# Kernel tuning notes

Hardware: AMD Instinct MI355X
Metric: run time of the kernel (lower is better)

The kernel has to match this reference:

```python
import jax, jax.numpy as jnp
import numpy as np

TOPK = 9
NUM_CLASSES = 80
BG_INDEX = NUM_CLASSES
B, N_GT = 16, 32
N_LEVEL_BBOXES = (25600, 6400, 1600)  # strides 8/16/32 on a 1280x1280 image
M = sum(N_LEVEL_BBOXES)
EPS = 1e-9


def _make_boxes(key, lead_shape, img_size=1280.0):
    k1, k2 = jax.random.split(key)
    c = jax.random.uniform(k1, lead_shape + (2,), minval=32.0, maxval=img_size - 32.0)
    wh = jax.random.uniform(k2, lead_shape + (2,), minval=8.0, maxval=256.0)
    return jnp.concatenate([c - wh * 0.5, c + wh * 0.5], axis=-1)


def setup_inputs() -> dict:
    key = jax.random.key(0)
    ks = jax.random.split(key, 5)
    anchor_bboxes = _make_boxes(ks[0], (M,))
    gt_bboxes = _make_boxes(ks[1], (B, N_GT))
    gt_labels = jax.random.randint(ks[2], (B, N_GT, 1), 0, NUM_CLASSES)
    mask_gt = (jax.random.uniform(ks[3], (B, N_GT, 1)) < 0.8).astype(jnp.float32)
    pred_bboxes = _make_boxes(ks[4], (B, M))
    return {"anchor_bboxes": anchor_bboxes, "n_level_bboxes": N_LEVEL_BBOXES,
            "gt_bboxes": gt_bboxes, "gt_labels": gt_labels,
            "mask_gt": mask_gt, "pred_bboxes": pred_bboxes}


def pairwise_iou(box1, box2):
    # box1 [..., N, 4], box2 [..., M, 4] -> [..., N, M]
    b1 = box1[..., :, None, :]
    b2 = box2[..., None, :, :]
    lt = jnp.maximum(b1[..., :2], b2[..., :2])
    rb = jnp.minimum(b1[..., 2:], b2[..., 2:])
    inter = jnp.clip(rb - lt, 0.0).prod(-1)
    area1 = (b1[..., 2:] - b1[..., :2]).prod(-1)
    area2 = (b2[..., 2:] - b2[..., :2]).prod(-1)
    return inter / (area1 + area2 - inter + EPS)


def reference(anchor_bboxes, n_level_bboxes, gt_bboxes, gt_labels, mask_gt, pred_bboxes):
    bs, n_max = gt_bboxes.shape[0], gt_bboxes.shape[1]
    n_anchors = anchor_bboxes.shape[0]

    overlaps = pairwise_iou(gt_bboxes.reshape(-1, 4), anchor_bboxes).reshape(bs, n_max, n_anchors)
    gt_centers = (gt_bboxes[..., :2] + gt_bboxes[..., 2:]) * 0.5            # [B,N,2]
    anchor_points = (anchor_bboxes[:, :2] + anchor_bboxes[:, 2:]) * 0.5      # [M,2]
    distances = jnp.sqrt(((gt_centers[:, :, None, :] - anchor_points[None, None, :, :]) ** 2).sum(-1))
    distances = jax.lax.stop_gradient(distances)  # only feeds integer topk indices

    # ---- per-FPN-level topk candidate selection (dedup via scatter-count) ----
    mask_gt_b = mask_gt.astype(bool)                 # [B,N,1]
    b_ix = jnp.arange(bs)[:, None, None]
    n_ix = jnp.arange(n_max)[None, :, None]
    is_in_candidate_list, candidate_indices = [], []
    start = 0
    for L in n_level_bboxes:
        k = min(TOPK, L)
        d = jax.lax.dynamic_slice_in_dim(distances, start, L, axis=-1)
        _, idx = jax.lax.top_k(-d, k)                # [B,N,k] k smallest distances
        candidate_indices.append(idx + start)
        idx_m = jnp.where(mask_gt_b, idx, 0)
        cnt = jnp.zeros((bs, n_max, L), distances.dtype).at[b_ix, n_ix, idx_m].add(1.0)
        cnt = jnp.where(cnt > 1, 0.0, cnt)           # drop duplicated indices
        is_in_candidate_list.append(cnt)
        start += L
    is_in_candidate = jnp.concatenate(is_in_candidate_list, -1)   # [B,N,M]
    candidate_indices = jnp.concatenate(candidate_indices, -1)    # [B,N,k*l]

    # ---- dynamic IoU threshold = mean + std over candidate overlaps ----
    iou_candidates = jnp.where(is_in_candidate > 0, overlaps, 0.0)
    gathered = jnp.take_along_axis(iou_candidates, candidate_indices, axis=-1)
    thr = gathered.mean(-1, keepdims=True) + gathered.std(-1, keepdims=True, ddof=1)
    is_positive = jnp.where(iou_candidates > thr, is_in_candidate, 0.0)

    # ---- anchor centers strictly inside gt boxes ----
    deltas = jnp.concatenate([anchor_points[None, None] - gt_bboxes[:, :, None, :2],
                              gt_bboxes[:, :, None, 2:] - anchor_points[None, None]], -1)
    is_in_gts = (deltas.min(-1) > EPS).astype(overlaps.dtype)     # [B,N,M]

    mask_positive = is_positive * is_in_gts * mask_gt

    # ---- resolve anchors matched to multiple gts by highest overlap ----
    fg_mask = mask_positive.sum(-2)                               # [B,M]
    multi = fg_mask[:, None, :] > 1
    is_max = jax.nn.one_hot(overlaps.argmax(1), n_max, dtype=mask_positive.dtype).transpose(0, 2, 1)
    mask_positive = jnp.where(multi, is_max, mask_positive)
    fg_mask = mask_positive.sum(-2)
    target_gt_index = mask_positive.argmax(-2)                    # [B,M]

    # ---- gather targets ----
    target_labels = jnp.take_along_axis(gt_labels[..., 0], target_gt_index, axis=1)
    target_labels = jnp.where(fg_mask > 0, target_labels, BG_INDEX)
    target_bboxes = jnp.take_along_axis(gt_bboxes, target_gt_index[..., None], axis=1)  # [B,M,4]
    target_scores = jax.nn.one_hot(target_labels, NUM_CLASSES + 1, dtype=jnp.float32)[..., :NUM_CLASSES]

    # ---- soft-label scaling by predicted-box IoU ----
    ious = pairwise_iou(gt_bboxes, pred_bboxes) * mask_positive
    target_scores = target_scores * ious.max(-2)[..., None]
    return target_labels, target_bboxes, target_scores, fg_mask > 0
```

## Files before the change

kernel.cpp:

```cpp
#include <hip/hip_runtime.h>
#include <stdint.h>

#define NCLS 80
#define BGI 80
#define BB 16
#define NGT 32
#define MM 33600
#define EPSF 1e-9f
#define CAP 1024

__device__ __forceinline__ float iou_f(const float4 b1, const float4 b2) {
#pragma clang fp contract(off)
  float ltx = fmaxf(b1.x, b2.x);
  float lty = fmaxf(b1.y, b2.y);
  float rbx = fminf(b1.z, b2.z);
  float rby = fminf(b1.w, b2.w);
  float iw = fmaxf(rbx - ltx, 0.0f);
  float ih = fmaxf(rby - lty, 0.0f);
  float inter = iw * ih;
  float a1 = (b1.z - b1.x) * (b1.w - b1.y);
  float a2 = (b2.z - b2.x) * (b2.w - b2.y);
  return inter / (a1 + a2 - inter + EPSF);
}

__global__ __launch_bounds__(256) void k_prep(
    const float4* __restrict__ anchors, float2* __restrict__ centers,
    unsigned int* __restrict__ pk) {
#pragma clang fp contract(off)
  const int i = blockIdx.x * 256 + threadIdx.x;
  if (i < MM) {
    const float4 ab = anchors[i];
    centers[i] = make_float2((ab.x + ab.z) * 0.5f, (ab.y + ab.w) * 0.5f);
  }
  pk[i] = 0u;
}

__global__ __launch_bounds__(1024) void k_topk(
    const float4* __restrict__ anchors, const float2* __restrict__ centers,
    const float4* __restrict__ gtb, const float* __restrict__ maskgt,
    unsigned int* __restrict__ pk) {
#pragma clang fp contract(off)
  const int pair = blockIdx.x;
  if (maskgt[pair] == 0.0f) return;
  const int b = pair >> 5;
  const int g = pair & 31;
  const int tid = threadIdx.x;
  const int lane = tid & 63;
  const int wid = tid >> 6;
  const float4 gb = gtb[pair];
  const float gcx = (gb.x + gb.z) * 0.5f;
  const float gcy = (gb.y + gb.w) * 0.5f;

  __shared__ unsigned long long buf[CAP];
  __shared__ unsigned long long winners[27];
  __shared__ float s_wmin[16];
  __shared__ float s_T;
  __shared__ unsigned int s_cnt;

  const int LSTART[3] = {0, 25600, 32000};
  const int LLEN[3]   = {25600, 6400, 1600};

#pragma unroll
  for (int lev = 0; lev < 3; ++lev) {
    const int start = LSTART[lev];
    const int len = LLEN[lev];

    float mymin = 3.4e38f;
    for (int j = tid; j < len; j += 1024) {
      const float2 ac = centers[start + j];
      const float dx = gcx - ac.x;
      const float dy = gcy - ac.y;
      mymin = fminf(mymin, dx * dx + dy * dy);
    }
#pragma unroll
    for (int s = 32; s >= 1; s >>= 1)
      mymin = fminf(mymin, __shfl_xor(mymin, s, 64));
    if (lane == 0) s_wmin[wid] = mymin;
    if (tid == 0) s_cnt = 0u;
    __syncthreads();

    if (wid == 0 && lane < 16) {
      const float v = s_wmin[lane];
      int r = 0;
#pragma unroll
      for (int q = 0; q < 16; ++q) {
        const float o = s_wmin[q];
        r += (o < v) || (o == v && q < lane);
      }
      if (r == 8) s_T = sqrtf(v);
    }
    __syncthreads();
    const float T = s_T;

    for (int j = tid; j < len; j += 1024) {
      const float2 ac = centers[start + j];
      const float dx = gcx - ac.x;
      const float dy = gcy - ac.y;
      const float dist = sqrtf(dx * dx + dy * dy);
      if (dist <= T) {
        const unsigned int p = atomicAdd(&s_cnt, 1u);
        if (p < CAP)
          buf[p] = ((unsigned long long)__float_as_uint(dist) << 32) |
                   (unsigned long long)(unsigned int)(start + j);
      }
    }
    __syncthreads();
    const int m = (int)min(s_cnt, (unsigned int)CAP);

    for (int i = tid; i < m; i += 1024) {
      const unsigned long long k = buf[i];
      int r = 0;
      for (int q = 0; q < m; ++q) r += (buf[q] < k);
      if (r < 9) winners[lev * 9 + r] = k;
    }
    __syncthreads();
  }

  if (wid != 0) return;

  unsigned int mycand = 0;
  if (lane < 27) mycand = (unsigned int)(winners[lane] & 0xffffffffu);

  float ov = 0.0f;
  bool inside = false;
  if (lane < 27) {
    const float4 ab = anchors[mycand];
    ov = iou_f(gb, ab);
    const float2 ac = centers[mycand];
    const float m1 = fminf(fminf(ac.x - gb.x, ac.y - gb.y),
                           fminf(gb.z - ac.x, gb.w - ac.y));
    inside = m1 > EPSF;
  }
  float s = (lane < 27) ? ov : 0.0f;
#pragma unroll
  for (int sft = 32; sft >= 1; sft >>= 1) s += __shfl_xor(s, sft, 64);
  const float mean = s / 27.0f;
  float dev = (lane < 27) ? (ov - mean) : 0.0f;
  float s2 = dev * dev;
#pragma unroll
  for (int sft = 32; sft >= 1; sft >>= 1) s2 += __shfl_xor(s2, sft, 64);
  const float thr = mean + sqrtf(s2 / 26.0f);

  if (lane < 27 && inside && ov > thr) {
    atomicAdd(&pk[b * MM + (int)mycand], (1u << 20) | (unsigned int)g);
  }
}

__global__ __launch_bounds__(320) void k_out(
    const float4* __restrict__ anchors, const float4* __restrict__ gtb,
    const int* __restrict__ glabels, const float4* __restrict__ predb,
    const unsigned int* __restrict__ pk,
    float* __restrict__ out_labels, float4* __restrict__ out_bbox,
    float* __restrict__ out_fg, float4* __restrict__ out_scores) {
  const int t = threadIdx.x;
  const int b = blockIdx.y;
  const int row0 = blockIdx.x * 64;

  __shared__ int s_lbl[64];
  __shared__ float s_iou[64];

  if (t < 64) {
    const int a = row0 + t;
    const int i = b * MM + a;
    const unsigned int p = pk[i];
    const unsigned int c = p >> 20;
    int g = 0;
    const bool fg = (c != 0u);
    if (c == 1u) {
      g = (int)(p & 0xFFFFFu);
    } else if (c > 1u) {
      const float4 ab = anchors[a];
      float best = -1.0f;
      for (int gg = 0; gg < NGT; ++gg) {
        const float ovv = iou_f(gtb[b * NGT + gg], ab);
        if (ovv > best) { best = ovv; g = gg; }
      }
    }
    const int lbl = fg ? glabels[b * NGT + g] : BGI;
    out_labels[i] = (float)lbl;
    out_bbox[i] = gtb[b * NGT + g];
    const float io = fg ? iou_f(gtb[b * NGT + g], predb[i]) : 0.0f;
    out_fg[i] = fg ? 1.0f : 0.0f;
    s_lbl[t] = fg ? lbl : -1;
    s_iou[t] = io;
  }
  __syncthreads();

  const size_t base = ((size_t)b * MM + row0) * 20;
#pragma unroll
  for (int it = 0; it < 4; ++it) {
    const int idx = it * 320 + t;
    const int row = idx / 20;
    const int c4 = idx - row * 20;
    const int lbl = s_lbl[row];
    const float io = s_iou[row];
    const int cb = c4 * 4;
    float4 v;
    v.x = (lbl == cb) ? io : 0.0f;
    v.y = (lbl == cb + 1) ? io : 0.0f;
    v.z = (lbl == cb + 2) ? io : 0.0f;
    v.w = (lbl == cb + 3) ? io : 0.0f;
    out_scores[base + idx] = v;
  }
}

extern "C" void kernel_launch(void* const* d_in, const int* in_sizes, int n_in,
                              void* d_out, int out_size, void* d_ws, size_t ws_size,
                              hipStream_t stream) {
  const float* anchors = nullptr;
  const float* gtb = nullptr;
  const int* glab = nullptr;
  const float* maskgt = nullptr;
  const float* predb = nullptr;
  int seen512 = 0;
  for (int i = 0; i < n_in; ++i) {
    const int sz = in_sizes[i];
    if (sz == 134400 && !anchors) anchors = (const float*)d_in[i];
    else if (sz == 2048 && !gtb) gtb = (const float*)d_in[i];
    else if (sz == 512) {
      if (seen512++ == 0) glab = (const int*)d_in[i];
      else maskgt = (const float*)d_in[i];
    } else if (sz == 2150400 && !predb) predb = (const float*)d_in[i];
  }
  if (!anchors || !gtb || !glab || !maskgt || !predb) return;

  float* out = (float*)d_out;
  float* out_labels = out;
  float4* out_bbox = (float4*)(out + 537600);
  float4* out_scores = (float4*)(out + 2688000);
  float* out_fg = out + 45696000;

  unsigned int* pk = (unsigned int*)d_ws;
  float2* centers = (float2*)(pk + 537600);

  k_prep<<<dim3(2100), dim3(256), 0, stream>>>(
      (const float4*)anchors, centers, pk);

  k_topk<<<dim3(BB * NGT), dim3(1024), 0, stream>>>(
      (const float4*)anchors, centers, (const float4*)gtb, maskgt, pk);

  k_out<<<dim3(525, BB), dim3(320), 0, stream>>>(
      (const float4*)anchors, (const float4*)gtb, glab, (const float4*)predb,
      pk, out_labels, out_bbox, out_fg, out_scores);
}
```

Baseline: 63.78 us.

## Zero score tensor inside topk kernel and scatter only foreground scores

Moves the bulk zero-fill of the dense target_scores tensor (B*M*80 floats) into the latency-bound topk kernel, interleaved with its reduction phases, so the memory writes overlap with the compute-bound candidate selection. The output kernel then writes only the single nonzero score per foreground anchor instead of the full 80-class row. This trades a write-heavy final kernel for extra store traffic in the topk blocks, which may slow their critical path. Correctness now depends on the zero-fill finishing before the scatter, which stream ordering guarantees.

```diff
diff --git a/kernel.cpp b/kernel.cpp
--- a/kernel.cpp
+++ b/kernel.cpp
@@ -8,6 +8,7 @@
 #define MM 33600
 #define EPSF 1e-9f
 #define CAP 1024
+#define ZPB 21000
 
 __device__ __forceinline__ float iou_f(const float4 b1, const float4 b2) {
 #pragma clang fp contract(off)
@@ -35,16 +36,34 @@
   pk[i] = 0u;
 }
 
+__device__ __forceinline__ void zstores(float4* __restrict__ zs,
+                                        const int base, const int site,
+                                        const int tid) {
+#pragma unroll
+  for (int it = 0; it < 7; ++it) {
+    const int idx = site * 7168 + it * 1024 + tid;
+    if (idx < ZPB) zs[base + idx] = make_float4(0.f, 0.f, 0.f, 0.f);
+  }
+}
+
 __global__ __launch_bounds__(1024) void k_topk(
     const float4* __restrict__ anchors, const float2* __restrict__ centers,
     const float4* __restrict__ gtb, const float* __restrict__ maskgt,
-    unsigned int* __restrict__ pk) {
+    unsigned int* __restrict__ pk, float4* __restrict__ zscores) {
 #pragma clang fp contract(off)
   const int pair = blockIdx.x;
-  if (maskgt[pair] == 0.0f) return;
+  const int tid = threadIdx.x;
+  const int zbase = pair * ZPB;
+
+  zstores(zscores, zbase, 0, tid);
+
+  if (maskgt[pair] == 0.0f) {
+    zstores(zscores, zbase, 1, tid);
+    zstores(zscores, zbase, 2, tid);
+    return;
+  }
   const int b = pair >> 5;
   const int g = pair & 31;
-  const int tid = threadIdx.x;
   const int lane = tid & 63;
   const int wid = tid >> 6;
   const float4 gb = gtb[pair];
@@ -78,6 +97,8 @@
     if (lane == 0) s_wmin[wid] = mymin;
     if (tid == 0) s_cnt = 0u;
     __syncthreads();
+
+    if (lev == 0) zstores(zscores, zbase, 1, tid);
 
     if (wid == 0 && lane < 16) {
       const float v = s_wmin[lane];
@@ -105,8 +126,10 @@
       }
     }
     __syncthreads();
+
+    if (lev == 0) zstores(zscores, zbase, 2, tid);
+
     const int m = (int)min(s_cnt, (unsigned int)CAP);
-
     for (int i = tid; i < m; i += 1024) {
       const unsigned long long k = buf[i];
       int r = 0;
@@ -146,61 +169,37 @@
   }
 }
 
-__global__ __launch_bounds__(320) void k_out(
+__global__ __launch_bounds__(256) void k_out(
     const float4* __restrict__ anchors, const float4* __restrict__ gtb,
     const int* __restrict__ glabels, const float4* __restrict__ predb,
     const unsigned int* __restrict__ pk,
     float* __restrict__ out_labels, float4* __restrict__ out_bbox,
-    float* __restrict__ out_fg, float4* __restrict__ out_scores) {
-  const int t = threadIdx.x;
+    float* __restrict__ out_fg, float* __restrict__ out_scores) {
+  const int a = blockIdx.x * 256 + threadIdx.x;
+  if (a >= MM) return;
   const int b = blockIdx.y;
-  const int row0 = blockIdx.x * 64;
-
-  __shared__ int s_lbl[64];
-  __shared__ float s_iou[64];
-
-  if (t < 64) {
-    const int a = row0 + t;
-    const int i = b * MM + a;
-    const unsigned int p = pk[i];
-    const unsigned int c = p >> 20;
-    int g = 0;
-    const bool fg = (c != 0u);
-    if (c == 1u) {
-      g = (int)(p & 0xFFFFFu);
-    } else if (c > 1u) {
-      const float4 ab = anchors[a];
-      float best = -1.0f;
-      for (int gg = 0; gg < NGT; ++gg) {
-        const float ovv = iou_f(gtb[b * NGT + gg], ab);
-        if (ovv > best) { best = ovv; g = gg; }
-      }
-    }
-    const int lbl = fg ? glabels[b * NGT + g] : BGI;
-    out_labels[i] = (float)lbl;
-    out_bbox[i] = gtb[b * NGT + g];
-    const float io = fg ? iou_f(gtb[b * NGT + g], predb[i]) : 0.0f;
-    out_fg[i] = fg ? 1.0f : 0.0f;
-    s_lbl[t] = fg ? lbl : -1;
-    s_iou[t] = io;
-  }
-  __syncthreads();
-
-  const size_t base = ((size_t)b * MM + row0) * 20;
-#pragma unroll
-  for (int it = 0; it < 4; ++it) {
-    const int idx = it * 320 + t;
-    const int row = idx / 20;
-    const int c4 = idx - row * 20;
-    const int lbl = s_lbl[row];
-    const float io = s_iou[row];
-    const int cb = c4 * 4;
-    float4 v;
-    v.x = (lbl == cb) ? io : 0.0f;
-    v.y = (lbl == cb + 1) ? io : 0.0f;
-    v.z = (lbl == cb + 2) ? io : 0.0f;
-    v.w = (lbl == cb + 3) ? io : 0.0f;
-    out_scores[base + idx] = v;
+  const int i = b * MM + a;
+  const unsigned int p = pk[i];
+  const unsigned int c = p >> 20;
+  int g = 0;
+  const bool fg = (c != 0u);
+  if (c == 1u) {
+    g = (int)(p & 0xFFFFFu);
+  } else if (c > 1u) {
+    const float4 ab = anchors[a];
+    float best = -1.0f;
+    for (int gg = 0; gg < NGT; ++gg) {
+      const float ovv = iou_f(gtb[b * NGT + gg], ab);
+      if (ovv > best) { best = ovv; g = gg; }
+    }
+  }
+  const int lbl = fg ? glabels[b * NGT + g] : BGI;
+  out_labels[i] = (float)lbl;
+  out_bbox[i] = gtb[b * NGT + g];
+  out_fg[i] = fg ? 1.0f : 0.0f;
+  if (fg) {
+    const float io = iou_f(gtb[b * NGT + g], predb[i]);
+    out_scores[(size_t)i * NCLS + lbl] = io;
   }
 }
 
@@ -227,7 +226,7 @@
   float* out = (float*)d_out;
   float* out_labels = out;
   float4* out_bbox = (float4*)(out + 537600);
-  float4* out_scores = (float4*)(out + 2688000);
+  float* out_scores = out + 2688000;
   float* out_fg = out + 45696000;
 
   unsigned int* pk = (unsigned int*)d_ws;
@@ -237,9 +236,10 @@
       (const float4*)anchors, centers, pk);
 
   k_topk<<<dim3(BB * NGT), dim3(1024), 0, stream>>>(
-      (const float4*)anchors, centers, (const float4*)gtb, maskgt, pk);
-
-  k_out<<<dim3(525, BB), dim3(320), 0, stream>>>(
+      (const float4*)anchors, centers, (const float4*)gtb, maskgt, pk,
+      (float4*)out_scores);
+
+  k_out<<<dim3(132, BB), dim3(256), 0, stream>>>(
       (const float4*)anchors, (const float4*)gtb, glab, (const float4*)predb,
       pk, out_labels, out_bbox, out_fg, out_scores);
 }
```

After: 59.38 us. 1.07x faster.
